# Kernel tuning notes

Hardware: AMD Instinct MI355X
Metric: run time of the kernel (lower is better)

## Reference

```python
import jax, jax.numpy as jnp
import numpy as np

B, S, V, D, H, KVH, L = 2, 1024, 8192, 1024, 16, 4, 8
HD = D // H          # 64, head dim
KV = KVH * HD        # 256, kv projection width
HID = 2736           # max(16, ceil(2*4*1024/48)*16)
NS = 4               # num_skip_weights = min(L//2, L - L//2)
SOFTCAP = 30.0
ROPE_BASE = 10000.0
RS_INIT = 1.0 / np.sqrt(L)


def setup_inputs() -> dict:
    key = jax.random.key(0)
    ks = iter(jax.random.split(key, 64))
    def rn(shape, s=0.02):
        return jax.random.normal(next(ks), shape, dtype=jnp.float32) * s
    inp = {}
    inp['idx'] = jax.random.randint(next(ks), (B, S), 0, V)
    inp['tok_emb'] = rn((V, D))
    inp['embed_norm_w'] = 1.0 + rn((D,))
    inp['resid_mix'] = jnp.stack([1.0 + rn((L, D), 0.05), rn((L, D), 0.05)], axis=1)  # [L,2,D]
    inp['attn_norm_w'] = 1.0 + rn((L, D))
    inp['mlp_norm_w'] = 1.0 + rn((L, D))
    inp['attn_scale'] = RS_INIT + rn((L, D))
    inp['mlp_scale'] = RS_INIT + rn((L, D))
    inp['Wq'] = rn((L, D, D))
    inp['Wk'] = rn((L, KV, D))
    inp['Wv'] = rn((L, KV, D))
    conv = lambda C: rn((L, 3, C), 0.1).at[:, 2, :].add(1.0)  # curr ~ 1, prev ~ 0
    inp['q_conv_w'] = conv(D)
    inp['k_conv_w'] = conv(KV)
    inp['v_conv_w'] = conv(KV)
    inp['q_gain'] = jnp.eye(H, dtype=jnp.float32)[None] + rn((L, H, H))
    inp['post_attn_norm_w'] = 1.0 + rn((L, D))
    inp['Wo'] = rn((L, D, D))
    inp['Wfc'] = rn((L, HID, D))
    inp['Wgate'] = rn((L, HID, D))
    inp['h_conv_w'] = rn((L, 3, HID), 0.1).at[:, 2, :].add(1.0)
    inp['h_norm_w'] = 1.0 + rn((L, HID))
    inp['Wmproj'] = rn((L, D, HID))
    inp['skip_weights'] = RS_INIT + rn((NS, D))
    inp['skip_gates'] = rn((NS, D), 0.1)
    inp['final_norm_w'] = 1.0 + rn((D,))
    inp['lm_head_w'] = rn((V, D))
    inp['bigram_head'] = rn((V, V))
    inp['bigram_scale'] = 0.02 + rn((V,), 0.005)
    inp['bigram_gate'] = rn((D,), 0.1)
    inp['unigram_bias'] = rn((V,), 0.01)
    return inp


def _rmsnorm(x, w=None):
    eps = jnp.finfo(x.dtype).eps
    y = x * jax.lax.rsqrt(jnp.mean(x * x, axis=-1, keepdims=True) + eps)
    return y * w if w is not None else y


def _dwconv(x, w):  # x [B,S,C], w [3,C]: causal depthwise 3-tap conv
    n = x.shape[1]
    xp = jnp.pad(x, ((0, 0), (2, 0), (0, 0)))
    return w[0] * xp[:, :n] + w[1] * xp[:, 1:n + 1] + w[2] * xp[:, 2:]


def _rope_tables(seqlen):
    inv_freq = 1.0 / (ROPE_BASE ** (jnp.arange(0, HD, 2, dtype=jnp.float32) / HD))
    freqs = jnp.outer(jnp.arange(seqlen, dtype=jnp.float32), inv_freq)  # [S, HD//2]
    return jnp.cos(freqs)[None, None], jnp.sin(freqs)[None, None]


def _apply_rope(x, cos, sin):
    half = x.shape[-1] // 2
    x1, x2 = x[..., :half], x[..., half:]
    return jnp.concatenate([x1 * cos + x2 * sin, -x1 * sin + x2 * cos], axis=-1)


def reference(idx, tok_emb, embed_norm_w, resid_mix, attn_norm_w, mlp_norm_w, attn_scale, mlp_scale, Wq, Wk, Wv, q_conv_w, k_conv_w, v_conv_w, q_gain, post_attn_norm_w, Wo, Wfc, Wgate, h_conv_w, h_norm_w, Wmproj, skip_weights, skip_gates, final_norm_w, lm_head_w, bigram_head, bigram_scale, bigram_gate, unigram_bias):
    cos, sin = _rope_tables(S)
    causal = jnp.tril(jnp.ones((S, S), dtype=bool))

    def attn(x, i):
        q = _dwconv(x @ Wq[i].T, q_conv_w[i]).reshape(B, S, H, HD).transpose(0, 2, 1, 3)
        k = _dwconv(x @ Wk[i].T, k_conv_w[i]).reshape(B, S, KVH, HD).transpose(0, 2, 1, 3)
        v = _dwconv(x @ Wv[i].T, v_conv_w[i]).reshape(B, S, KVH, HD).transpose(0, 2, 1, 3)
        q = _apply_rope(_rmsnorm(q), cos, sin)
        k = _apply_rope(_rmsnorm(k), cos, sin)
        q = jnp.einsum('hg,bgsd->bhsd', q_gain[i], q)
        kr = jnp.repeat(k, H // KVH, axis=1)
        vr = jnp.repeat(v, H // KVH, axis=1)
        scores = jnp.einsum('bhsd,bhtd->bhst', q, kr) / np.sqrt(HD).astype(np.float32)
        scores = jnp.where(causal, scores, -jnp.inf)
        p = jax.nn.softmax(scores, axis=-1)
        y = jnp.einsum('bhst,bhtd->bhsd', p, vr).transpose(0, 2, 1, 3).reshape(B, S, D)
        return _rmsnorm(y, post_attn_norm_w[i]) @ Wo[i].T

    def mlp(x, i):
        h = (x @ Wfc[i].T) * jax.nn.silu(x @ Wgate[i].T)
        h = _rmsnorm(_dwconv(h, h_conv_w[i]), h_norm_w[i])
        return h @ Wmproj[i].T

    def block(x, x0, i):
        x = resid_mix[i, 0] * x + resid_mix[i, 1] * x0
        x = x + attn_scale[i] * attn(_rmsnorm(x, attn_norm_w[i]), i)
        x = x + mlp_scale[i] * mlp(_rmsnorm(x, mlp_norm_w[i]), i)
        return x

    x = _rmsnorm(tok_emb[idx], embed_norm_w)
    x0 = x
    enc = L // 2
    skips = []
    for i in range(enc):
        x = block(x, x0, i)
        skips.append(x)
    for j in range(L - enc):
        if j < NS:
            x = x + (skip_weights[j] * jax.nn.sigmoid(skip_gates[j]))[None, None, :] * skips.pop()
        x = block(x, x0, enc + j)
    x = _rmsnorm(x, final_norm_w)

    logits = x @ lm_head_w.T + unigram_bias
    gate = jax.nn.sigmoid(x @ bigram_gate)[..., None]        # [B,S,1]
    logits = logits + gate * (bigram_head[idx] * bigram_scale)
    return SOFTCAP * jnp.tanh(logits / SOFTCAP)
```

## Files before the change

### kernel.cpp

```cpp
#include <hip/hip_runtime.h>
#include <hip/hip_bf16.h>
#include <cstdint>
#include <cstddef>

#define B_   2
#define S_   1024
#define V_   8192
#define D_   1024
#define H_   16
#define KVH_ 4
#define L_   8
#define HD_  64
#define KV_  256
#define HID_ 2736
#define HIDP 2752
#define NT_  (B_*S_)
#define EPSF 1.1920928955078125e-7f
#define SOFTCAPF 30.0f

typedef __bf16 bf8 __attribute__((ext_vector_type(8)));
typedef __bf16 bf4 __attribute__((ext_vector_type(4)));
typedef float  f4  __attribute__((ext_vector_type(4)));

#define GLDS16(g, l) __builtin_amdgcn_global_load_lds( \
    (const __attribute__((address_space(1))) void*)(g), \
    (__attribute__((address_space(3))) void*)(l), 16, 0, 0)

__device__ __forceinline__ float wsum(float v){
#pragma unroll
  for (int m = 32; m >= 1; m >>= 1) v += __shfl_xor(v, m, 64);
  return v;
}
__device__ __forceinline__ float blocksum256(float v){
  __shared__ float red[4];
  v = wsum(v);
  if ((threadIdx.x & 63) == 0) red[threadIdx.x >> 6] = v;
  __syncthreads();
  return red[0] + red[1] + red[2] + red[3];
}
__device__ __forceinline__ float4 ld4b(const __bf16* p, size_t i4){
  bf4 v = ((const bf4*)p)[i4];
  return make_float4((float)v[0], (float)v[1], (float)v[2], (float)v[3]);
}

template<int BM, int BN, int OUT>
__global__ __launch_bounds__(256) void k_gemm(
    const __bf16* __restrict__ A, const __bf16* __restrict__ Wt,
    void* __restrict__ Cv, int M, int N, int K, int lda, int mtiles)
{
  constexpr int SMEM = (BM + BN) * 128;
  __shared__ __attribute__((aligned(16))) unsigned char smem[SMEM];
  __bf16* As = (__bf16*)smem;
  __bf16* Bs = (__bf16*)(smem + BM*128);

  const int tid  = threadIdx.x;
  const int nwg = gridDim.x;
  const int wg  = (blockIdx.x & 7) * (nwg >> 3) + (blockIdx.x >> 3);
  const int bm   = wg % mtiles;
  const int bn   = wg / mtiles;
  const int m0   = bm * BM, n0 = bn * BN;
  const int lane = tid & 63, wv = tid >> 6;
  const int wm   = (wv >> 1) * (BM / 2);
  const int wn   = (wv & 1) * (BN / 2);
  const int fr   = lane & 15, g = lane >> 4;
  constexpr int MI = BM / 32;
  constexpr int NJ = BN / 32;
  constexpr int AP = BM / 32;
  constexpr int BP = BN / 32;

  f4 acc[MI][NJ] = {};

  const int rs = lane >> 3, ss = lane & 7;
  const int cseg = ss ^ ((wv*8 + rs) & 7);
  const __bf16* aq[AP];
#pragma unroll
  for (int p = 0; p < AP; ++p)
    aq[p] = A + (size_t)(m0 + wv*8 + p*32 + rs) * lda + cseg*8;
  const __bf16* bq[BP];
#pragma unroll
  for (int p = 0; p < BP; ++p) {
    int rB = n0 + wv*8 + p*32 + rs; if (rB > N-1) rB = N-1;
    bq[p] = Wt + (size_t)rB * K + cseg*8;
  }

  for (int k0 = 0; k0 < K; k0 += 64) {
    __syncthreads();
#pragma unroll
    for (int p = 0; p < AP; ++p) GLDS16(aq[p] + k0, As + (wv*8 + p*32)*64);
#pragma unroll
    for (int p = 0; p < BP; ++p) GLDS16(bq[p] + k0, Bs + (wv*8 + p*32)*64);
    __syncthreads();

#pragma unroll
    for (int ks = 0; ks < 2; ++ks) {
      const int sgo = (((ks*4 + g) ^ (fr & 7)) << 3);
      bf8 af[MI], bf[NJ];
#pragma unroll
      for (int i = 0; i < MI; ++i)
        af[i] = *(const bf8*)&As[(wm + i*16 + fr)*64 + sgo];
#pragma unroll
      for (int j = 0; j < NJ; ++j)
        bf[j] = *(const bf8*)&Bs[(wn + j*16 + fr)*64 + sgo];
#pragma unroll
      for (int i = 0; i < MI; ++i)
#pragma unroll
        for (int j = 0; j < NJ; ++j)
          acc[i][j] = __builtin_amdgcn_mfma_f32_16x16x32_bf16(af[i], bf[j], acc[i][j], 0, 0, 0);
    }
  }

  const int rbase = g << 2;
#pragma unroll
  for (int i = 0; i < MI; ++i) {
    int gm = m0 + wm + i*16 + rbase;
#pragma unroll
    for (int j = 0; j < NJ; ++j) {
      int gn = n0 + wn + j*16 + fr;
      if (gn < N) {
        if constexpr (OUT == 1) {
#pragma unroll
          for (int r = 0; r < 4; ++r)
            ((__bf16*)Cv)[(size_t)(gm + r) * N + gn] = (__bf16)acc[i][j][r];
        } else {
#pragma unroll
          for (int r = 0; r < 4; ++r)
            ((float*)Cv)[(size_t)(gm + r) * N + gn] = acc[i][j][r];
        }
      }
    }
  }
}

#define STG8(t, h, b) do { \
    if ((h) < 2) { \
      const __bf16* _s = A + (size_t)(m0 + (h)*128 + w16 + rsub) * lda + (t)*32 + sseg*8; \
      GLDS16(_s, smem + (b)*32768 + ((h)*128 + w16) * 64); \
    } else { \
      int _rB = n0 + ((h)-2)*128 + w16 + rsub; if (_rB > N-1) _rB = N-1; \
      const __bf16* _s = Wt + (size_t)_rB * K + (t)*32 + sseg*8; \
      GLDS16(_s, smem + (b)*32768 + 16384 + (((h)-2)*128 + w16) * 64); \
    } } while (0)

#define LDA8(b, r, gg) (*(const bf8*)(smem + (b)*32768 + (r)*64 + (((gg) ^ ((((r)>>3)&1)<<1)))*16))
#define LDB8(b, r, gg) (*(const bf8*)(smem + (b)*32768 + 16384 + (r)*64 + (((gg) ^ ((((r)>>3)&1)<<1)))*16))

#define PH8(bt, q, dostage, st, sh, sb, W) do { \
    const int _r0 = wr*128 + ((q)>>1)*64 + fr; \
    const int _c0 = wc*64 + ((q)&1)*32 + fr; \
    bf8 _a0 = LDA8(bt, _r0 +  0, g); \
    bf8 _a1 = LDA8(bt, _r0 + 16, g); \
    bf8 _a2 = LDA8(bt, _r0 + 32, g); \
    bf8 _a3 = LDA8(bt, _r0 + 48, g); \
    bf8 _b0 = LDB8(bt, _c0 +  0, g); \
    bf8 _b1 = LDB8(bt, _c0 + 16, g); \
    if (dostage) STG8(st, sh, sb); \
    if ((W) == 4)      asm volatile("s_waitcnt vmcnt(4)" ::: "memory"); \
    else if ((W) == 0) asm volatile("s_waitcnt vmcnt(0)" ::: "memory"); \
    asm volatile("" ::: "memory"); \
    __builtin_amdgcn_s_barrier(); \
    asm volatile("" ::: "memory"); \
    __builtin_amdgcn_s_setprio(1); \
    acc[((q)>>1)*4+0][((q)&1)*2+0] = __builtin_amdgcn_mfma_f32_16x16x32_bf16(_a0, _b0, acc[((q)>>1)*4+0][((q)&1)*2+0], 0,0,0); \
    acc[((q)>>1)*4+0][((q)&1)*2+1] = __builtin_amdgcn_mfma_f32_16x16x32_bf16(_a0, _b1, acc[((q)>>1)*4+0][((q)&1)*2+1], 0,0,0); \
    acc[((q)>>1)*4+1][((q)&1)*2+0] = __builtin_amdgcn_mfma_f32_16x16x32_bf16(_a1, _b0, acc[((q)>>1)*4+1][((q)&1)*2+0], 0,0,0); \
    acc[((q)>>1)*4+1][((q)&1)*2+1] = __builtin_amdgcn_mfma_f32_16x16x32_bf16(_a1, _b1, acc[((q)>>1)*4+1][((q)&1)*2+1], 0,0,0); \
    acc[((q)>>1)*4+2][((q)&1)*2+0] = __builtin_amdgcn_mfma_f32_16x16x32_bf16(_a2, _b0, acc[((q)>>1)*4+2][((q)&1)*2+0], 0,0,0); \
    acc[((q)>>1)*4+2][((q)&1)*2+1] = __builtin_amdgcn_mfma_f32_16x16x32_bf16(_a2, _b1, acc[((q)>>1)*4+2][((q)&1)*2+1], 0,0,0); \
    acc[((q)>>1)*4+3][((q)&1)*2+0] = __builtin_amdgcn_mfma_f32_16x16x32_bf16(_a3, _b0, acc[((q)>>1)*4+3][((q)&1)*2+0], 0,0,0); \
    acc[((q)>>1)*4+3][((q)&1)*2+1] = __builtin_amdgcn_mfma_f32_16x16x32_bf16(_a3, _b1, acc[((q)>>1)*4+3][((q)&1)*2+1], 0,0,0); \
    __builtin_amdgcn_s_setprio(0); \
    asm volatile("" ::: "memory"); \
    __builtin_amdgcn_s_barrier(); \
    asm volatile("" ::: "memory"); \
  } while (0)

template<int OUT>
__global__ __launch_bounds__(512, 2) void k_gemm8(
    const __bf16* __restrict__ A, const __bf16* __restrict__ Wt,
    void* __restrict__ Cv, int M, int N, int K, int lda, int mtiles,
    const int* __restrict__ idx, const float* __restrict__ gateb,
    const float* __restrict__ bhd, const float* __restrict__ bsc,
    const float* __restrict__ ub)
{
  __shared__ __attribute__((aligned(16))) unsigned char smem[98304];
  const int tid = threadIdx.x;
  const int nwg = gridDim.x;
  const int wg  = (blockIdx.x & 7) * (nwg >> 3) + (blockIdx.x >> 3);
  const int bm = wg % mtiles, bnn = wg / mtiles;
  const int m0 = bm << 8, n0 = bnn << 8;
  const int l = tid & 63, wid = tid >> 6;
  const int wr = wid >> 2, wc = wid & 3;
  const int fr = l & 15, g = l >> 4;

  f4 acc[8][4] = {};

  const int w16  = wid * 16;
  const int rsub = l >> 2;
  const int sseg = (l & 3) ^ ((l >= 32) ? 2 : 0);

  const int nk = K >> 5;
  const int ni = nk >> 1;

  STG8(0, 0, 0); STG8(0, 1, 0); STG8(0, 2, 0); STG8(0, 3, 0);
  STG8(1, 0, 1); STG8(1, 1, 1); STG8(1, 2, 1); STG8(1, 3, 1);
  asm volatile("s_waitcnt vmcnt(4)" ::: "memory");
  asm volatile("" ::: "memory");
  __builtin_amdgcn_s_barrier();
  asm volatile("" ::: "memory");

  int b0 = 0;
  for (int i = 0; i < ni; ++i) {
    const int b1 = (b0 == 2) ? 0 : b0 + 1;
    const int b2 = (b1 == 2) ? 0 : b1 + 1;
    const bool nlast = (i + 1 < ni);
    const int t2 = 2*i + 2, t3 = 2*i + 3;
    PH8(b0, 0, nlast, t2, 0, b2, -1);
    PH8(b0, 1, nlast, t2, 1, b2, -1);
    PH8(b0, 2, nlast, t2, 2, b2, -1);
    PH8(b0, 3, nlast, t2, 3, b2, nlast ? 4 : 0);
    PH8(b1, 0, nlast, t3, 0, b0, -1);
    PH8(b1, 1, nlast, t3, 1, b0, -1);
    PH8(b1, 2, nlast, t3, 2, b0, -1);
    PH8(b1, 3, nlast, t3, 3, b0, nlast ? 4 : -1);
    b0 = b2;
  }

  if constexpr (OUT == 1) {
    __bf16* C = (__bf16*)Cv;
#pragma unroll
    for (int ii = 0; ii < 8; ++ii) {
      int gm = m0 + wr*128 + ii*16 + g*4;
#pragma unroll
      for (int j = 0; j < 4; ++j) {
        int gn = n0 + wc*64 + j*16 + fr;
        if (gn < N) {
#pragma unroll
          for (int r = 0; r < 4; ++r)
            C[(size_t)(gm + r) * N + gn] = (__bf16)acc[ii][j][r];
        }
      }
    }
  } else {
    float* EP = (float*)smem;
    __syncthreads();
#pragma unroll
    for (int pass = 0; pass < 4; ++pass) {
      if (wr == (pass >> 1)) {
#pragma unroll
        for (int a = 0; a < 4; ++a) {
          int ii = (pass & 1)*4 + a;
#pragma unroll
          for (int j = 0; j < 4; ++j)
#pragma unroll
            for (int r = 0; r < 4; ++r)
              EP[(a*16 + g*4 + r)*256 + wc*64 + j*16 + fr] = acc[ii][j][r];
        }
      }
      __syncthreads();
#pragma unroll
      for (int it = 0; it < 8; ++it) {
        int row = it*8 + (tid >> 6);
        int c0  = (tid & 63) << 2;
        int grow = m0 + pass*64 + row;
        int gn = n0 + c0;
        float gt = gateb[grow];
        int tk = idx[grow];
        float4 a4 = *(float4*)&EP[row*256 + c0];
        float4 b4 = *(const float4*)&bhd[(size_t)tk * V_ + gn];
        float4 u4 = *(const float4*)&ub[gn];
        float4 s4 = *(const float4*)&bsc[gn];
        float4 o;
        o.x = SOFTCAPF * tanhf((a4.x + u4.x + gt*b4.x*s4.x) / SOFTCAPF);
        o.y = SOFTCAPF * tanhf((a4.y + u4.y + gt*b4.y*s4.y) / SOFTCAPF);
        o.z = SOFTCAPF * tanhf((a4.z + u4.z + gt*b4.z*s4.z) / SOFTCAPF);
        o.w = SOFTCAPF * tanhf((a4.w + u4.w + gt*b4.w*s4.w) / SOFTCAPF);
        *(float4*)&((float*)Cv)[(size_t)grow * N + gn] = o;
      }
      __syncthreads();
    }
  }
}
#undef PH8
#undef LDA8
#undef LDB8
#undef STG8

__global__ void k_cvt(const float* __restrict__ s, __bf16* __restrict__ d,
                      int perL, int K, int Kpad, long dstL, long dstOff, long nd4)
{
  long i = (long)blockIdx.x * 256 + threadIdx.x;
  if (i >= nd4) return;
  const int kp4 = Kpad >> 2;
  long row = i / kp4;
  int  c   = (int)(i % kp4) << 2;
  long layer = row / perL, r = row % perL;
  bf4 o;
  if (c < K) {
    float4 v = *(const float4*)(s + (layer*perL + r) * (long)K + c);
    o[0] = (__bf16)v.x; o[1] = (__bf16)v.y; o[2] = (__bf16)v.z; o[3] = (__bf16)v.w;
  } else { o[0] = o[1] = o[2] = o[3] = (__bf16)0.f; }
  *(bf4*)(d + layer*dstL + dstOff + (long)r*Kpad + c) = o;
}

__global__ void k_embed(const int* __restrict__ idx, const float* __restrict__ emb,
                        const float* __restrict__ wn, float* __restrict__ x, float* __restrict__ x0)
{
  const int r = blockIdx.x, t = threadIdx.x;
  const float4 v = ((const float4*)(emb + (size_t)idx[r] * D_))[t];
  float ss = blocksum256(v.x*v.x + v.y*v.y + v.z*v.z + v.w*v.w);
  float rs = rsqrtf(ss / (float)D_ + EPSF);
  const float4 w = ((const float4*)wn)[t];
  float4 o = make_float4(v.x*rs*w.x, v.y*rs*w.y, v.z*rs*w.z, v.w*rs*w.w);
  ((float4*)(x  + (size_t)r * D_))[t] = o;
  ((float4*)(x0 + (size_t)r * D_))[t] = o;
}

__global__ void k_blockstart(
    float* __restrict__ x, const float* __restrict__ x0,
    const __bf16* __restrict__ t1, const float* __restrict__ msc,
    float* __restrict__ skstore, const float* __restrict__ skread, int same,
    const float* __restrict__ skw, const float* __restrict__ skg,
    const float* __restrict__ mix, const float* __restrict__ nw,
    __bf16* __restrict__ xn)
{
  const int r = blockIdx.x, t = threadIdx.x;
  const size_t i4 = (size_t)r * 256 + t;
  float4 xv = ((float4*)x)[i4];
  if (t1) {
    float4 tv = ld4b(t1, i4);
    float4 s  = ((const float4*)msc)[t];
    xv.x += s.x*tv.x; xv.y += s.y*tv.y; xv.z += s.z*tv.z; xv.w += s.w*tv.w;
  }
  if (skstore) ((float4*)skstore)[i4] = xv;
  if (skw) {
    float4 sv;
    if (same) sv = xv;
    else      sv = ((const float4*)skread)[i4];
    float4 w = ((const float4*)skw)[t];
    float4 g = ((const float4*)skg)[t];
    xv.x += w.x / (1.f + __expf(-g.x)) * sv.x;
    xv.y += w.y / (1.f + __expf(-g.y)) * sv.y;
    xv.z += w.z / (1.f + __expf(-g.z)) * sv.z;
    xv.w += w.w / (1.f + __expf(-g.w)) * sv.w;
  }
  float4 x0v = ((const float4*)x0)[i4];
  float4 m0  = ((const float4*)mix)[t];
  float4 m1  = ((const float4*)(mix + D_))[t];
  float4 nv;
  nv.x = m0.x*xv.x + m1.x*x0v.x; nv.y = m0.y*xv.y + m1.y*x0v.y;
  nv.z = m0.z*xv.z + m1.z*x0v.z; nv.w = m0.w*xv.w + m1.w*x0v.w;
  ((float4*)x)[i4] = nv;
  float ss = blocksum256(nv.x*nv.x + nv.y*nv.y + nv.z*nv.z + nv.w*nv.w);
  float rs = rsqrtf(ss / (float)D_ + EPSF);
  const float4 w = ((const float4*)nw)[t];
  bf4 o = { (__bf16)(nv.x*rs*w.x), (__bf16)(nv.y*rs*w.y),
            (__bf16)(nv.z*rs*w.z), (__bf16)(nv.w*rs*w.w) };
  ((bf4*)xn)[i4] = o;
}

__global__ void k_addnorm(float* __restrict__ x, const __bf16* __restrict__ t1,
                          const float* __restrict__ sc, const float* __restrict__ nw,
                          __bf16* __restrict__ xn,
                          const float* __restrict__ bg, float* __restrict__ gateb)
{
  const int r = blockIdx.x, t = threadIdx.x;
  const size_t i4 = (size_t)r * 256 + t;
  float4 xv = ((float4*)x)[i4];
  float4 tv = ld4b(t1, i4);
  float4 s  = ((const float4*)sc)[t];
  xv.x += s.x*tv.x; xv.y += s.y*tv.y; xv.z += s.z*tv.z; xv.w += s.w*tv.w;
  ((float4*)x)[i4] = xv;
  float ss = blocksum256(xv.x*xv.x + xv.y*xv.y + xv.z*xv.z + xv.w*xv.w);
  float rs = rsqrtf(ss / (float)D_ + EPSF);
  const float4 w = ((const float4*)nw)[t];
  float ox = xv.x*rs*w.x, oy = xv.y*rs*w.y, oz = xv.z*rs*w.z, ow = xv.w*rs*w.w;
  bf4 o = { (__bf16)ox, (__bf16)oy, (__bf16)oz, (__bf16)ow };
  ((bf4*)xn)[i4] = o;
  if (bg) {
    float4 b4 = ((const float4*)bg)[t];
    float gd = ox*b4.x + oy*b4.y + oz*b4.z + ow*b4.w;
    __syncthreads();
    float gs = blocksum256(gd);
    if (t == 0) gateb[r] = 1.f / (1.f + __expf(-gs));
  }
}

__global__ void k_rmsnormb(const float* __restrict__ in, const float* __restrict__ w,
                           __bf16* __restrict__ out)
{
  const int r = blockIdx.x, t = threadIdx.x;
  float4 v = ((const float4*)(in + (size_t)r * D_))[t];
  float ss = blocksum256(v.x*v.x + v.y*v.y + v.z*v.z + v.w*v.w);
  float rs = rsqrtf(ss / (float)D_ + EPSF);
  const float4 w4 = ((const float4*)w)[t];
  bf4 o = { (__bf16)(v.x*rs*w4.x), (__bf16)(v.y*rs*w4.y),
            (__bf16)(v.z*rs*w4.z), (__bf16)(v.w*rs*w4.w) };
  ((bf4*)(out + (size_t)r * D_))[t] = o;
}

__device__ __forceinline__ float conv3b(const __bf16* buf, int tok, int s, int ld, int col,
                                        const float* w, int C, int c){
  const __bf16* p0 = buf + (size_t)tok * ld + col;
  float a  = (s >= 2) ? (float)p0[-2*ld] : 0.f;
  float bb = (s >= 1) ? (float)p0[-ld]   : 0.f;
  return w[c]*a + w[C + c]*bb + w[2*C + c]*(float)p0[0];
}

__global__ __launch_bounds__(256) void k_prep(
    const __bf16* __restrict__ qkv,
    const float* __restrict__ qcw, const float* __restrict__ kcw, const float* __restrict__ vcw,
    const float* __restrict__ qgain,
    __bf16* __restrict__ q2, __bf16* __restrict__ k2, __bf16* __restrict__ v2)
{
  const int tok = blockIdx.x;
  const int s = tok & (S_ - 1);
  const int t = threadIdx.x, lane = t & 63, w = t >> 6;
  __shared__ float qsh[1024];

  const int j = lane & 31;
  float freq = __expf(-(float)j * (9.210340371976184f / 32.f));
  float sn, cs;
  __sincosf((float)s * freq, &sn, &cs);

#pragma unroll
  for (int k = 0; k < 4; ++k) {
    int c = t + k*256;
    float qc = conv3b(qkv, tok, s, 1536, c, qcw, D_, c);
    float ssq = wsum(qc * qc);
    float qn = qc * rsqrtf(ssq / 64.f + EPSF);
    float pr = __shfl_xor(qn, 32, 64);
    qsh[c] = qn * cs + ((lane < 32) ? pr * sn : -pr * sn);
  }
  __syncthreads();
  float qg[16];
#pragma unroll
  for (int g = 0; g < 16; ++g) qg[g] = qsh[g*64 + lane];
#pragma unroll
  for (int k = 0; k < 4; ++k) {
    int h = (k << 2) + w;
    float acc = 0.f;
#pragma unroll
    for (int g = 0; g < 16; ++g) acc += qgain[h*16 + g] * qg[g];
    q2[(size_t)tok * D_ + h*64 + lane] = (__bf16)acc;
  }

  {
    float kc = conv3b(qkv, tok, s, 1536, 1024 + t, kcw, KV_, t);
    float ssk = wsum(kc * kc);
    float kn = kc * rsqrtf(ssk / 64.f + EPSF);
    float pk = __shfl_xor(kn, 32, 64);
    k2[(size_t)tok * KV_ + t] = (__bf16)(kn * cs + ((lane < 32) ? pk * sn : -pk * sn));
  }
  v2[(size_t)tok * KV_ + t] = (__bf16)conv3b(qkv, tok, s, 1536, 1280 + t, vcw, KV_, t);
}

#define LDK 72
__global__ __launch_bounds__(256) void k_attn(
    const __bf16* __restrict__ q2, const __bf16* __restrict__ k2,
    const __bf16* __restrict__ v2, float* __restrict__ y)
{
  __shared__ __attribute__((aligned(16))) __bf16 Ks[64*LDK];
  __shared__ __attribute__((aligned(16))) __bf16 Vt[64*LDK];
  __shared__ __attribute__((aligned(16))) __bf16 Ps[4][16*LDK];

  const int id = blockIdx.x;
  const int h  = (id >> 4) & 15;
  const int b  = id >> 8;
  const int qb = b ? (15 - (id & 15)) : (id & 15);
  const int tid = threadIdx.x, l = tid & 63, wq = tid >> 6;
  const int g = l >> 4, fr = l & 15;
  const int kvh = h >> 2;
  const int qrow = qb*64 + wq*16 + fr;

  bf8 qf[2];
#pragma unroll
  for (int ks = 0; ks < 2; ++ks)
    qf[ks] = *(const bf8*)&q2[(size_t)(b*S_ + qrow)*D_ + h*64 + g*8 + ks*32];

  float m = -1e30f, lsum = 0.f;
  f4 acc[4] = {};

  const int nch = qb + 1;
  for (int ch = 0; ch < nch; ++ch) {
    const int t0 = ch << 6;
    __syncthreads();
#pragma unroll
    for (int it = 0; it < 2; ++it) {
      int i = tid + it*256;
      int row = i >> 3, seg = (i & 7) << 3;
      *(bf8*)&Ks[row*LDK + seg] =
        *(const bf8*)&k2[(size_t)(b*S_ + t0 + row)*KV_ + kvh*64 + seg];
    }
    {
      int key4 = (tid & 15) << 2, hd4 = (tid >> 4) << 2;
      bf4 vv[4];
#pragma unroll
      for (int kk = 0; kk < 4; ++kk)
        vv[kk] = *(const bf4*)&v2[(size_t)(b*S_ + t0 + key4 + kk)*KV_ + kvh*64 + hd4];
#pragma unroll
      for (int hh = 0; hh < 4; ++hh) {
        bf4 w = { vv[0][hh], vv[1][hh], vv[2][hh], vv[3][hh] };
        *(bf4*)&Vt[(hd4 + hh)*LDK + key4] = w;
      }
    }
    __syncthreads();

    f4 sc[4] = {};
#pragma unroll
    for (int ks = 0; ks < 2; ++ks)
#pragma unroll
      for (int t = 0; t < 4; ++t) {
        bf8 kf = *(const bf8*)&Ks[(t*16 + fr)*LDK + g*8 + ks*32];
        sc[t] = __builtin_amdgcn_mfma_f32_16x16x32_bf16(kf, qf[ks], sc[t], 0, 0, 0);
      }

    const bool lastch = (ch == qb);
    float s[4][4];
    float pmax = -1e30f;
#pragma unroll
    for (int t = 0; t < 4; ++t)
#pragma unroll
      for (int r = 0; r < 4; ++r) {
        float v = sc[t][r] * 0.125f;
        if (lastch && (t0 + t*16 + g*4 + r > qrow)) v = -1e30f;
        s[t][r] = v;
        pmax = fmaxf(pmax, v);
      }
    pmax = fmaxf(pmax, __shfl_xor(pmax, 16, 64));
    pmax = fmaxf(pmax, __shfl_xor(pmax, 32, 64));
    float mnew = fmaxf(m, pmax);
    float alpha = __expf(m - mnew);
    float rs = 0.f;
#pragma unroll
    for (int t = 0; t < 4; ++t)
#pragma unroll
      for (int r = 0; r < 4; ++r) { float p = __expf(s[t][r] - mnew); s[t][r] = p; rs += p; }
    rs += __shfl_xor(rs, 16, 64);
    rs += __shfl_xor(rs, 32, 64);
    lsum = lsum * alpha + rs;
    m = mnew;
#pragma unroll
    for (int t = 0; t < 4; ++t) acc[t] = acc[t] * alpha;

#pragma unroll
    for (int t = 0; t < 4; ++t) {
      bf4 pw = { (__bf16)s[t][0], (__bf16)s[t][1], (__bf16)s[t][2], (__bf16)s[t][3] };
      *(bf4*)&Ps[wq][fr*LDK + t*16 + g*4] = pw;
    }

#pragma unroll
    for (int ks = 0; ks < 2; ++ks) {
      bf8 pf = *(const bf8*)&Ps[wq][fr*LDK + g*8 + ks*32];
#pragma unroll
      for (int t = 0; t < 4; ++t) {
        bf8 vf = *(const bf8*)&Vt[(t*16 + fr)*LDK + g*8 + ks*32];
        acc[t] = __builtin_amdgcn_mfma_f32_16x16x32_bf16(vf, pf, acc[t], 0, 0, 0);
      }
    }
  }

  float inv = 1.f / lsum;
#pragma unroll
  for (int t = 0; t < 4; ++t)
#pragma unroll
    for (int r = 0; r < 4; ++r)
      y[(size_t)(b*S_ + qrow)*D_ + h*64 + t*16 + g*4 + r] = acc[t][r] * inv;
}

__device__ __forceinline__ float hprodb(const __bf16* row, int c){
  float a = (float)row[c], b = (float)row[HID_ + c];
  return a * b / (1.f + __expf(-b));
}
__global__ __launch_bounds__(256) void k_hfuse(
    const __bf16* __restrict__ hb, const float* __restrict__ cw,
    const float* __restrict__ nw, __bf16* __restrict__ out)
{
  const int tok = blockIdx.x, t = threadIdx.x;
  const int s = tok & (S_ - 1);
  const __bf16* row0 = hb + (size_t)tok * 5472;
  float v[11]; float ss = 0.f;
#pragma unroll
  for (int ii = 0; ii < 11; ++ii) {
    int c = t + ii*256;
    float cv = 0.f;
    if (c < HID_) {
      float p0 = hprodb(row0, c);
      float p1 = (s >= 1) ? hprodb(row0 - 5472, c) : 0.f;
      float p2 = (s >= 2) ? hprodb(row0 - 2*5472, c) : 0.f;
      cv = cw[c]*p2 + cw[HID_ + c]*p1 + cw[2*HID_ + c]*p0;
    }
    v[ii] = cv; ss += cv*cv;
  }
  ss = blocksum256(ss);
  float rs = rsqrtf(ss / (float)HID_ + EPSF);
#pragma unroll
  for (int ii = 0; ii < 11; ++ii) {
    int c = t + ii*256;
    if (c < HIDP)
      out[(size_t)tok * HIDP + c] = (c < HID_) ? (__bf16)(v[ii]*rs*nw[c]) : (__bf16)0.f;
  }
}

template<int BM, int BN, int OUT>
static inline void gemm(const __bf16* A, const __bf16* W, void* C, int M, int N, int K,
                        int lda, hipStream_t s)
{
  int mt = M / BM, nt = (N + BN - 1) / BN;
  k_gemm<BM, BN, OUT><<<dim3(mt * nt), dim3(256), 0, s>>>(A, W, C, M, N, K, lda, mt);
}

template<int OUT>
static inline void gemm8(const __bf16* A, const __bf16* W, void* C, int M, int N, int K,
                         int lda, hipStream_t s,
                         const int* idx = nullptr, const float* gateb = nullptr,
                         const float* bhd = nullptr, const float* bsc = nullptr,
                         const float* ub = nullptr)
{
  int mt = M >> 8, nt = (N + 255) >> 8;
  k_gemm8<OUT><<<dim3(mt * nt), dim3(512), 0, s>>>(A, W, C, M, N, K, lda, mt,
                                                   idx, gateb, bhd, bsc, ub);
}

extern "C" void kernel_launch(void* const* d_in, const int* in_sizes, int n_in,
                              void* d_out, int out_size, void* d_ws, size_t ws_size,
                              hipStream_t stream)
{
  const int*   idx    = (const int*)d_in[0];
  const float* temb   = (const float*)d_in[1];
  const float* enw    = (const float*)d_in[2];
  const float* rmix   = (const float*)d_in[3];
  const float* anw    = (const float*)d_in[4];
  const float* mnw    = (const float*)d_in[5];
  const float* ascale = (const float*)d_in[6];
  const float* mscale = (const float*)d_in[7];
  const float* Wq     = (const float*)d_in[8];
  const float* Wk     = (const float*)d_in[9];
  const float* Wv     = (const float*)d_in[10];
  const float* qcw    = (const float*)d_in[11];
  const float* kcw    = (const float*)d_in[12];
  const float* vcw    = (const float*)d_in[13];
  const float* qgain  = (const float*)d_in[14];
  const float* panw   = (const float*)d_in[15];
  const float* Wo     = (const float*)d_in[16];
  const float* Wfc    = (const float*)d_in[17];
  const float* Wgate  = (const float*)d_in[18];
  const float* hcw    = (const float*)d_in[19];
  const float* hnw    = (const float*)d_in[20];
  const float* Wmp    = (const float*)d_in[21];
  const float* skw    = (const float*)d_in[22];
  const float* skg    = (const float*)d_in[23];
  const float* fnw    = (const float*)d_in[24];
  const float* lmw    = (const float*)d_in[25];
  const float* bh     = (const float*)d_in[26];
  const float* bsc    = (const float*)d_in[27];
  const float* bg     = (const float*)d_in[28];
  const float* ub     = (const float*)d_in[29];

  float* p = (float*)d_ws;
  float* x    = p; p += (size_t)NT_ * D_;
  float* x0   = p; p += (size_t)NT_ * D_;
  float* y    = p; p += (size_t)NT_ * D_;
  float* skips= p; p += (size_t)4 * NT_ * D_;
  float* gateb= p; p += NT_;
  __bf16* qkvb= (__bf16*)p; p += (size_t)NT_ * 1536 / 2;
  __bf16* hbb = (__bf16*)p; p += (size_t)NT_ * 5472 / 2;
  __bf16* t1b = (__bf16*)p; p += (size_t)NT_ * D_ / 2;
  __bf16* xnb = (__bf16*)p; p += (size_t)NT_ * D_ / 2;
  __bf16* q2b = (__bf16*)p; p += (size_t)NT_ * D_ / 2;
  __bf16* k2b = (__bf16*)p; p += (size_t)NT_ * KV_ / 2;
  __bf16* v2b = (__bf16*)p; p += (size_t)NT_ * KV_ / 2;
  __bf16* hnb = (__bf16*)p; p += (size_t)NT_ * HIDP / 2;
  __bf16* wqkv= (__bf16*)p; p += (size_t)L_ * 1536 * 1024 / 2;
  __bf16* wob = (__bf16*)p; p += (size_t)L_ * 1024 * 1024 / 2;
  __bf16* wfcg= (__bf16*)p; p += (size_t)L_ * 5472 * 1024 / 2;
  __bf16* wmpb= (__bf16*)p; p += (size_t)L_ * 1024 * HIDP / 2;
  __bf16* wlmb= (__bf16*)p; p += (size_t)V_ * 1024 / 2;
  float* logits = (float*)d_out;

  auto cvt = [&](const float* s, __bf16* d, int perL, int K, int Kpad,
                 long dstL, long dstOff, int nl) {
    long nd4 = (long)nl * perL * (Kpad >> 2);
    int grid = (int)((nd4 + 255) / 256);
    k_cvt<<<grid, 256, 0, stream>>>(s, d, perL, K, Kpad, dstL, dstOff, nd4);
  };
  cvt(Wq,    wqkv, 1024, 1024, 1024, 1536L*1024, 0,          L_);
  cvt(Wk,    wqkv,  256, 1024, 1024, 1536L*1024, 1024L*1024, L_);
  cvt(Wv,    wqkv,  256, 1024, 1024, 1536L*1024, 1280L*1024, L_);
  cvt(Wo,    wob,  1024, 1024, 1024, 1024L*1024, 0,          L_);
  cvt(Wfc,   wfcg, 2736, 1024, 1024, 5472L*1024, 0,          L_);
  cvt(Wgate, wfcg, 2736, 1024, 1024, 5472L*1024, 2736L*1024, L_);
  cvt(Wmp,   wmpb, 1024, 2736, HIDP, 1024L*HIDP, 0,          L_);
  cvt(lmw,   wlmb, 8192, 1024, 1024, 8192L*1024, 0,          1);

  k_embed<<<NT_, 256, 0, stream>>>(idx, temb, enw, x, x0);

  for (int i = 0; i < L_; ++i) {
    const float* pmsc = (i > 0) ? mscale + (size_t)(i-1) * D_ : nullptr;
    float* skst = (i >= 1 && i <= 4) ? skips + (size_t)(i-1) * NT_ * D_ : nullptr;
    const float* skrd = (i >= 4) ? skips + (size_t)(7-i) * NT_ * D_ : nullptr;
    const float* swp = (i >= 4) ? skw + (size_t)(i-4) * D_ : nullptr;
    const float* sgp = (i >= 4) ? skg + (size_t)(i-4) * D_ : nullptr;
    k_blockstart<<<NT_, 256, 0, stream>>>(x, x0, (i > 0) ? t1b : nullptr, pmsc,
                                          skst, skrd, (i == 4) ? 1 : 0, swp, sgp,
                                          rmix + (size_t)i * 2 * D_,
                                          anw + (size_t)i * D_, xnb);
    gemm<64, 128, 1>(xnb, wqkv + (size_t)i * 1536 * 1024, qkvb, NT_, 1536, 1024, 1024, stream);
    k_prep<<<NT_, 256, 0, stream>>>(qkvb,
                                    qcw + (size_t)i * 3 * D_, kcw + (size_t)i * 3 * KV_,
                                    vcw + (size_t)i * 3 * KV_, qgain + (size_t)i * H_ * H_,
                                    q2b, k2b, v2b);
    k_attn<<<B_ * H_ * (S_/64), 256, 0, stream>>>(q2b, k2b, v2b, y);
    k_rmsnormb<<<NT_, 256, 0, stream>>>(y, panw + (size_t)i * D_, xnb);
    gemm<64, 64, 1>(xnb, wob + (size_t)i * 1024 * 1024, t1b, NT_, 1024, 1024, 1024, stream);
    k_addnorm<<<NT_, 256, 0, stream>>>(x, t1b, ascale + (size_t)i * D_,
                                       mnw + (size_t)i * D_, xnb, nullptr, nullptr);
    gemm8<1>(xnb, wfcg + (size_t)i * 5472 * 1024, hbb, NT_, 5472, 1024, 1024, stream);
    k_hfuse<<<NT_, 256, 0, stream>>>(hbb, hcw + (size_t)i * 3 * HID_,
                                     hnw + (size_t)i * HID_, hnb);
    gemm<64, 64, 1>(hnb, wmpb + (size_t)i * 1024 * HIDP, t1b, NT_, 1024, HIDP, HIDP, stream);
  }

  k_addnorm<<<NT_, 256, 0, stream>>>(x, t1b, mscale + (size_t)7 * D_, fnw, xnb, bg, gateb);
  gemm8<2>(xnb, wlmb, logits, NT_, V_, 1024, 1024, stream, idx, gateb, bh, bsc, ub);
}
```

Before: 1.906 ms.

## Split-K by two for QKV, out-proj and MLP down-proj GEMMs with fused partial sums

Adds a split-K template parameter to the generic GEMM. With SK=2, each workgroup computes half of the K range and writes a bf16 partial into one of two output buffers, and the grid is doubled. The downstream consumers (k_prep's causal conv, k_blockstart, k_addnorm) now read both partials and add them, so no separate reduction kernel is needed. HIDP is padded to 2816 so that half of K stays a multiple of the 64-wide K tile. The aim is more workgroups and better CU occupancy for these small-N GEMMs. The cost is extra partial-output traffic, an additional bf16 rounding per partial, and more reads in the elementwise kernels.

```diff
diff --git a/kernel.cpp b/kernel.cpp
--- a/kernel.cpp
+++ b/kernel.cpp
@@ -13,7 +13,7 @@
 #define HD_  64
 #define KV_  256
 #define HID_ 2736
-#define HIDP 2752
+#define HIDP 2816
 #define NT_  (B_*S_)
 #define EPSF 1.1920928955078125e-7f
 #define SOFTCAPF 30.0f
@@ -43,7 +43,7 @@
   return make_float4((float)v[0], (float)v[1], (float)v[2], (float)v[3]);
 }
 
-template<int BM, int BN, int OUT>
+template<int BM, int BN, int OUT, int SK>
 __global__ __launch_bounds__(256) void k_gemm(
     const __bf16* __restrict__ A, const __bf16* __restrict__ Wt,
     void* __restrict__ Cv, int M, int N, int K, int lda, int mtiles)
@@ -56,9 +56,13 @@
   const int tid  = threadIdx.x;
   const int nwg = gridDim.x;
   const int wg  = (blockIdx.x & 7) * (nwg >> 3) + (blockIdx.x >> 3);
-  const int bm   = wg % mtiles;
-  const int bn   = wg / mtiles;
+  const int kz   = (SK == 2) ? (wg & 1) : 0;
+  const int wgt  = (SK == 2) ? (wg >> 1) : wg;
+  const int bm   = wgt % mtiles;
+  const int bn   = wgt / mtiles;
   const int m0   = bm * BM, n0 = bn * BN;
+  const int Keff = K / SK;
+  const int koff = kz * Keff;
   const int lane = tid & 63, wv = tid >> 6;
   const int wm   = (wv >> 1) * (BM / 2);
   const int wn   = (wv & 1) * (BN / 2);
@@ -75,15 +79,15 @@
   const __bf16* aq[AP];
 #pragma unroll
   for (int p = 0; p < AP; ++p)
-    aq[p] = A + (size_t)(m0 + wv*8 + p*32 + rs) * lda + cseg*8;
+    aq[p] = A + (size_t)(m0 + wv*8 + p*32 + rs) * lda + koff + cseg*8;
   const __bf16* bq[BP];
 #pragma unroll
   for (int p = 0; p < BP; ++p) {
     int rB = n0 + wv*8 + p*32 + rs; if (rB > N-1) rB = N-1;
-    bq[p] = Wt + (size_t)rB * K + cseg*8;
-  }
-
-  for (int k0 = 0; k0 < K; k0 += 64) {
+    bq[p] = Wt + (size_t)rB * K + koff + cseg*8;
+  }
+
+  for (int k0 = 0; k0 < Keff; k0 += 64) {
     __syncthreads();
 #pragma unroll
     for (int p = 0; p < AP; ++p) GLDS16(aq[p] + k0, As + (wv*8 + p*32)*64);
@@ -110,6 +114,7 @@
   }
 
   const int rbase = g << 2;
+  __bf16* Cb = (__bf16*)Cv + (size_t)kz * M * N;
 #pragma unroll
   for (int i = 0; i < MI; ++i) {
     int gm = m0 + wm + i*16 + rbase;
@@ -117,15 +122,9 @@
     for (int j = 0; j < NJ; ++j) {
       int gn = n0 + wn + j*16 + fr;
       if (gn < N) {
-        if constexpr (OUT == 1) {
-#pragma unroll
-          for (int r = 0; r < 4; ++r)
-            ((__bf16*)Cv)[(size_t)(gm + r) * N + gn] = (__bf16)acc[i][j][r];
-        } else {
-#pragma unroll
-          for (int r = 0; r < 4; ++r)
-            ((float*)Cv)[(size_t)(gm + r) * N + gn] = acc[i][j][r];
-        }
+#pragma unroll
+        for (int r = 0; r < 4; ++r)
+          Cb[(size_t)(gm + r) * N + gn] = (__bf16)acc[i][j][r];
       }
     }
   }
@@ -317,7 +316,8 @@
 
 __global__ void k_blockstart(
     float* __restrict__ x, const float* __restrict__ x0,
-    const __bf16* __restrict__ t1, const float* __restrict__ msc,
+    const __bf16* __restrict__ t1, const __bf16* __restrict__ t1p2,
+    const float* __restrict__ msc,
     float* __restrict__ skstore, const float* __restrict__ skread, int same,
     const float* __restrict__ skw, const float* __restrict__ skg,
     const float* __restrict__ mix, const float* __restrict__ nw,
@@ -328,8 +328,10 @@
   float4 xv = ((float4*)x)[i4];
   if (t1) {
     float4 tv = ld4b(t1, i4);
+    float4 t2 = ld4b(t1p2, i4);
     float4 s  = ((const float4*)msc)[t];
-    xv.x += s.x*tv.x; xv.y += s.y*tv.y; xv.z += s.z*tv.z; xv.w += s.w*tv.w;
+    xv.x += s.x*(tv.x + t2.x); xv.y += s.y*(tv.y + t2.y);
+    xv.z += s.z*(tv.z + t2.z); xv.w += s.w*(tv.w + t2.w);
   }
   if (skstore) ((float4*)skstore)[i4] = xv;
   if (skw) {
@@ -359,6 +361,7 @@
 }
 
 __global__ void k_addnorm(float* __restrict__ x, const __bf16* __restrict__ t1,
+                          const __bf16* __restrict__ t1p2,
                           const float* __restrict__ sc, const float* __restrict__ nw,
                           __bf16* __restrict__ xn,
                           const float* __restrict__ bg, float* __restrict__ gateb)
@@ -367,8 +370,10 @@
   const size_t i4 = (size_t)r * 256 + t;
   float4 xv = ((float4*)x)[i4];
   float4 tv = ld4b(t1, i4);
+  float4 t2 = ld4b(t1p2, i4);
   float4 s  = ((const float4*)sc)[t];
-  xv.x += s.x*tv.x; xv.y += s.y*tv.y; xv.z += s.z*tv.z; xv.w += s.w*tv.w;
+  xv.x += s.x*(tv.x + t2.x); xv.y += s.y*(tv.y + t2.y);
+  xv.z += s.z*(tv.z + t2.z); xv.w += s.w*(tv.w + t2.w);
   ((float4*)x)[i4] = xv;
   float ss = blocksum256(xv.x*xv.x + xv.y*xv.y + xv.z*xv.z + xv.w*xv.w);
   float rs = rsqrtf(ss / (float)D_ + EPSF);
@@ -398,16 +403,19 @@
   ((bf4*)(out + (size_t)r * D_))[t] = o;
 }
 
-__device__ __forceinline__ float conv3b(const __bf16* buf, int tok, int s, int ld, int col,
-                                        const float* w, int C, int c){
-  const __bf16* p0 = buf + (size_t)tok * ld + col;
-  float a  = (s >= 2) ? (float)p0[-2*ld] : 0.f;
-  float bb = (s >= 1) ? (float)p0[-ld]   : 0.f;
-  return w[c]*a + w[C + c]*bb + w[2*C + c]*(float)p0[0];
+__device__ __forceinline__ float conv3b2(const __bf16* bA, const __bf16* bB,
+                                         int tok, int s, int ld, int col,
+                                         const float* w, int C, int c){
+  const __bf16* pA = bA + (size_t)tok * ld + col;
+  const __bf16* pB = bB + (size_t)tok * ld + col;
+  float a  = (s >= 2) ? ((float)pA[-2*ld] + (float)pB[-2*ld]) : 0.f;
+  float bb = (s >= 1) ? ((float)pA[-ld]   + (float)pB[-ld])   : 0.f;
+  float cc = (float)pA[0] + (float)pB[0];
+  return w[c]*a + w[C + c]*bb + w[2*C + c]*cc;
 }
 
 __global__ __launch_bounds__(256) void k_prep(
-    const __bf16* __restrict__ qkv,
+    const __bf16* __restrict__ qkv, const __bf16* __restrict__ qkv2,
     const float* __restrict__ qcw, const float* __restrict__ kcw, const float* __restrict__ vcw,
     const float* __restrict__ qgain,
     __bf16* __restrict__ q2, __bf16* __restrict__ k2, __bf16* __restrict__ v2)
@@ -425,7 +433,7 @@
 #pragma unroll
   for (int k = 0; k < 4; ++k) {
     int c = t + k*256;
-    float qc = conv3b(qkv, tok, s, 1536, c, qcw, D_, c);
+    float qc = conv3b2(qkv, qkv2, tok, s, 1536, c, qcw, D_, c);
     float ssq = wsum(qc * qc);
     float qn = qc * rsqrtf(ssq / 64.f + EPSF);
     float pr = __shfl_xor(qn, 32, 64);
@@ -445,13 +453,13 @@
   }
 
   {
-    float kc = conv3b(qkv, tok, s, 1536, 1024 + t, kcw, KV_, t);
+    float kc = conv3b2(qkv, qkv2, tok, s, 1536, 1024 + t, kcw, KV_, t);
     float ssk = wsum(kc * kc);
     float kn = kc * rsqrtf(ssk / 64.f + EPSF);
     float pk = __shfl_xor(kn, 32, 64);
     k2[(size_t)tok * KV_ + t] = (__bf16)(kn * cs + ((lane < 32) ? pk * sn : -pk * sn));
   }
-  v2[(size_t)tok * KV_ + t] = (__bf16)conv3b(qkv, tok, s, 1536, 1280 + t, vcw, KV_, t);
+  v2[(size_t)tok * KV_ + t] = (__bf16)conv3b2(qkv, qkv2, tok, s, 1536, 1280 + t, vcw, KV_, t);
 }
 
 #define LDK 72
@@ -601,12 +609,12 @@
   }
 }
 
-template<int BM, int BN, int OUT>
+template<int BM, int BN, int OUT, int SK>
 static inline void gemm(const __bf16* A, const __bf16* W, void* C, int M, int N, int K,
                         int lda, hipStream_t s)
 {
   int mt = M / BM, nt = (N + BN - 1) / BN;
-  k_gemm<BM, BN, OUT><<<dim3(mt * nt), dim3(256), 0, s>>>(A, W, C, M, N, K, lda, mt);
+  k_gemm<BM, BN, OUT, SK><<<dim3(mt * nt * SK), dim3(256), 0, s>>>(A, W, C, M, N, K, lda, mt);
 }
 
 template<int OUT>
@@ -662,9 +670,9 @@
   float* y    = p; p += (size_t)NT_ * D_;
   float* skips= p; p += (size_t)4 * NT_ * D_;
   float* gateb= p; p += NT_;
-  __bf16* qkvb= (__bf16*)p; p += (size_t)NT_ * 1536 / 2;
+  __bf16* qkvb= (__bf16*)p; p += (size_t)2 * NT_ * 1536 / 2;
   __bf16* hbb = (__bf16*)p; p += (size_t)NT_ * 5472 / 2;
-  __bf16* t1b = (__bf16*)p; p += (size_t)NT_ * D_ / 2;
+  __bf16* t1b = (__bf16*)p; p += (size_t)2 * NT_ * D_ / 2;
   __bf16* xnb = (__bf16*)p; p += (size_t)NT_ * D_ / 2;
   __bf16* q2b = (__bf16*)p; p += (size_t)NT_ * D_ / 2;
   __bf16* k2b = (__bf16*)p; p += (size_t)NT_ * KV_ / 2;
@@ -676,6 +684,9 @@
   __bf16* wmpb= (__bf16*)p; p += (size_t)L_ * 1024 * HIDP / 2;
   __bf16* wlmb= (__bf16*)p; p += (size_t)V_ * 1024 / 2;
   float* logits = (float*)d_out;
+
+  const __bf16* qkvb2 = qkvb + (size_t)NT_ * 1536;
+  const __bf16* t1b2  = t1b + (size_t)NT_ * D_;
 
   auto cvt = [&](const float* s, __bf16* d, int perL, int K, int Kpad,
                  long dstL, long dstOff, int nl) {
@@ -700,26 +711,26 @@
     const float* skrd = (i >= 4) ? skips + (size_t)(7-i) * NT_ * D_ : nullptr;
     const float* swp = (i >= 4) ? skw + (size_t)(i-4) * D_ : nullptr;
     const float* sgp = (i >= 4) ? skg + (size_t)(i-4) * D_ : nullptr;
-    k_blockstart<<<NT_, 256, 0, stream>>>(x, x0, (i > 0) ? t1b : nullptr, pmsc,
+    k_blockstart<<<NT_, 256, 0, stream>>>(x, x0, (i > 0) ? t1b : nullptr, t1b2, pmsc,
                                           skst, skrd, (i == 4) ? 1 : 0, swp, sgp,
                                           rmix + (size_t)i * 2 * D_,
                                           anw + (size_t)i * D_, xnb);
-    gemm<64, 128, 1>(xnb, wqkv + (size_t)i * 1536 * 1024, qkvb, NT_, 1536, 1024, 1024, stream);
-    k_prep<<<NT_, 256, 0, stream>>>(qkvb,
+    gemm<64, 128, 1, 2>(xnb, wqkv + (size_t)i * 1536 * 1024, qkvb, NT_, 1536, 1024, 1024, stream);
+    k_prep<<<NT_, 256, 0, stream>>>(qkvb, qkvb2,
                                     qcw + (size_t)i * 3 * D_, kcw + (size_t)i * 3 * KV_,
                                     vcw + (size_t)i * 3 * KV_, qgain + (size_t)i * H_ * H_,
                                     q2b, k2b, v2b);
     k_attn<<<B_ * H_ * (S_/64), 256, 0, stream>>>(q2b, k2b, v2b, y);
     k_rmsnormb<<<NT_, 256, 0, stream>>>(y, panw + (size_t)i * D_, xnb);
-    gemm<64, 64, 1>(xnb, wob + (size_t)i * 1024 * 1024, t1b, NT_, 1024, 1024, 1024, stream);
-    k_addnorm<<<NT_, 256, 0, stream>>>(x, t1b, ascale + (size_t)i * D_,
+    gemm<64, 64, 1, 2>(xnb, wob + (size_t)i * 1024 * 1024, t1b, NT_, 1024, 1024, 1024, stream);
+    k_addnorm<<<NT_, 256, 0, stream>>>(x, t1b, t1b2, ascale + (size_t)i * D_,
                                        mnw + (size_t)i * D_, xnb, nullptr, nullptr);
     gemm8<1>(xnb, wfcg + (size_t)i * 5472 * 1024, hbb, NT_, 5472, 1024, 1024, stream);
     k_hfuse<<<NT_, 256, 0, stream>>>(hbb, hcw + (size_t)i * 3 * HID_,
                                      hnw + (size_t)i * HID_, hnb);
-    gemm<64, 64, 1>(hnb, wmpb + (size_t)i * 1024 * HIDP, t1b, NT_, 1024, HIDP, HIDP, stream);
-  }
-
-  k_addnorm<<<NT_, 256, 0, stream>>>(x, t1b, mscale + (size_t)7 * D_, fnw, xnb, bg, gateb);
+    gemm<64, 64, 1, 2>(hnb, wmpb + (size_t)i * 1024 * HIDP, t1b, NT_, 1024, HIDP, HIDP, stream);
+  }
+
+  k_addnorm<<<NT_, 256, 0, stream>>>(x, t1b, t1b2, mscale + (size_t)7 * D_, fnw, xnb, bg, gateb);
   gemm8<2>(xnb, wlmb, logits, NT_, V_, 1024, 1024, stream, idx, gateb, bh, bsc, ub);
 }
```

Result: faster. 1.683 ms (-11.7%).
